# Optimization experiments

Measured on AMD Instinct MI355X. Metric: run time of the kernel, lower is better.

The kernel has to match this reference:

```python
import jax, jax.numpy as jnp
import numpy as np

NEG = -1.0e30  # log-space 'zero' that is safe in fp32
EPS = 1e-7     # keras.backend.ctc_batch_cost epsilon


def setup_inputs() -> dict:
    key = jax.random.key(0)
    k1, k2 = jax.random.split(key)
    B, T, C, L = 256, 512, 256, 128
    # y_pred are post-softmax probabilities, as expected by ctc_batch_cost
    logits = jax.random.normal(k1, (B, T, C), dtype=jnp.float32)
    y_pred = jax.nn.softmax(logits, axis=-1)
    # labels in [0, C-1): never equal to blank index C-1
    y_true = jax.random.randint(k2, (B, L), 0, C - 1, dtype=jnp.int32)
    return {"y_true": y_true, "y_pred": y_pred}


def _ctc_batch_cost(y_true, y_pred):
    """Faithful keras.backend.ctc_batch_cost with full input/label lengths.

    y_true: [B, L] int labels (no blanks). y_pred: [B, T, C] probabilities.
    Blank index = C - 1 (TF v1 ctc_loss convention). Returns [B, 1] loss.
    """
    B, T, C = y_pred.shape
    L = y_true.shape[1]
    blank = C - 1
    S = 2 * L + 1  # extended label: blank, l0, blank, l1, ..., blank

    logp = jnp.log(y_pred + EPS)                                # [B, T, C]
    ext = jnp.full((B, S), blank, dtype=y_true.dtype).at[:, 1::2].set(y_true)
    # per-(t, s) log prob of the extended symbol
    lp = jnp.take_along_axis(logp, ext[:, None, :].astype(jnp.int32), axis=2)  # [B, T, S]

    # skip transition s-2 -> s allowed iff s >= 2, ext[s] != blank, ext[s] != ext[s-2]
    ext_m2 = jnp.pad(ext, ((0, 0), (2, 0)), constant_values=blank)[:, :S]
    skip = (ext != blank) & (ext != ext_m2) & (jnp.arange(S)[None, :] >= 2)

    # alpha init at t=0: only s=0 (blank) and s=1 (first label) reachable
    alpha0 = jnp.where(jnp.arange(S)[None, :] < 2, lp[:, 0, :], NEG)  # [B, S]

    def step(alpha, lp_t):
        p1 = jnp.pad(alpha, ((0, 0), (1, 0)), constant_values=NEG)[:, :S]
        p2 = jnp.pad(alpha, ((0, 0), (2, 0)), constant_values=NEG)[:, :S]
        a = jnp.logaddexp(alpha, p1)
        a = jnp.logaddexp(a, jnp.where(skip, p2, NEG))
        return a + lp_t, None

    lp_time_major = jnp.moveaxis(lp, 1, 0)  # [T, B, S]
    alpha, _ = jax.lax.scan(step, alpha0, lp_time_major[1:])
    # total log-likelihood ends at last blank or last label
    loss = -jnp.logaddexp(alpha[:, S - 1], alpha[:, S - 2])    # [B]
    return loss[:, None]                                        # [B, 1]


def reference(y_true, y_pred):
    # CTCLayer.call computes ctc_batch_cost with input_length = T, label_length = L
    # for every batch row, adds it as a loss, and passes y_pred through. The
    # compute of interest is the loss itself, returned here as [B, 1].
    return _ctc_batch_cost(y_true, y_pred)
```

## Files before the change

kernel.cpp:

```cpp
#include <hip/hip_runtime.h>
#include <math.h>


namespace {
constexpr int Bn = 256;
constexpr int Tn = 512;
constexpr int Cn = 256;
constexpr int Ln = 128;
constexpr int D  = 32;
constexpr float EPSf = 1e-7f;
constexpr float LN2f = 0.69314718055994530942f;
constexpr int   TGT  = 100;
}

typedef float f4 __attribute__((ext_vector_type(4)));

#define GLOAD(dst, p) \
    asm volatile("global_load_dwordx4 %0, %1, off" : "=v"(dst) : "v"(p))
#define WAITP(dst) \
    asm volatile("s_waitcnt vmcnt(31)" : "+v"(dst))
#define WAIT0(dst) \
    asm volatile("s_waitcnt vmcnt(0)" : "+v"(dst))

__device__ __forceinline__ float rdl63(float v) {
    return __int_as_float(__builtin_amdgcn_readlane(__float_as_int(v), 63));
}

__global__ __launch_bounds__(64, 1)
void ctc_fwd(const int* __restrict__ y_true,
             const float* __restrict__ y_pred,
             float* __restrict__ out)
{
    const int b    = blockIdx.x;
    const int lane = threadIdx.x;

    __shared__ __align__(16) float lds[4 * Cn];

    const int* yt = y_true + b * Ln;
    const int l0 = yt[2 * lane];
    const int l1 = yt[2 * lane + 1];
    const int lm = (lane > 0) ? yt[2 * lane - 1] : -1;
    const float sk1 = (lane > 0 && l0 != lm) ? 1.0f : 0.0f;
    const float sk3 = (l1 != l0) ? 1.0f : 0.0f;
    const float lzm = (lane > 0) ? 1.0f : 0.0f;

    float a0 = (lane == 0) ? 0x1p100f : 0.0f;
    float a1 = 0.0f, a2 = 0.0f, a3 = 0.0f, a4 = 0.0f;
    int Eacc = -100;

    auto step = [&](float rb, float r0, float r1) {
        float n = __shfl_up(a3, 1) * lzm;
        const float Pb = rb + EPSf;
        const float P0 = r0 + EPSf;
        const float P1 = r1 + EPSf;
        const float na0 = (a0 + n) * Pb;
        const float na1 = fmaf(sk1, n,  a1 + a0) * P0;
        const float na2 = (a2 + a1) * Pb;
        const float na3 = fmaf(sk3, a1, a3 + a2) * P1;
        const float na4 = (a4 + a3) * Pb;
        a0 = na0; a1 = na1; a2 = na2; a3 = na3; a4 = na4;
    };

    auto rescale = [&]() {
        float m = fmaxf(fmaxf(fmaxf(a0, a1), fmaxf(a2, a3)), a4);
        #pragma unroll
        for (int off = 32; off >= 1; off >>= 1)
            m = fmaxf(m, __shfl_xor(m, off));
        int e;
        (void)frexpf(m, &e);
        const int shift = TGT - e;
        a0 = ldexpf(a0, shift);
        a1 = ldexpf(a1, shift);
        a2 = ldexpf(a2, shift);
        a3 = ldexpf(a3, shift);
        a4 = ldexpf(a4, shift);
        Eacc -= shift;
    };

    const f4* p = (const f4*)(y_pred + (size_t)b * Tn * Cn) + lane;
    f4 buf[D];
    #pragma unroll
    for (int j = 0; j < D; ++j) { GLOAD(buf[j], p); p += Cn / 4; }

    float bold = 0.0f;

    #pragma unroll
    for (int j = 0; j < D; ++j) {
        WAITP(buf[j]);
        const float bnew = rdl63(buf[j].w);
        float r0n = 0.0f, r1n = 0.0f;
        if (j >= 1) {
            r0n = lds[((j - 1) & 3) * Cn + l0];
            r1n = lds[((j - 1) & 3) * Cn + l1];
        }
        ((f4*)lds)[(j & 3) * (Cn / 4) + lane] = buf[j];
        GLOAD(buf[j], p); p += Cn / 4;
        if (j >= 1) step(bold, r0n, r1n);
        bold = bnew;
        if (j == 16) rescale();
    }

    for (int c = D; c < Tn - D; c += D) {
        #pragma unroll
        for (int j = 0; j < D; ++j) {
            WAITP(buf[j]);
            const float bnew = rdl63(buf[j].w);
            const float r0n = lds[((j - 1) & 3) * Cn + l0];
            const float r1n = lds[((j - 1) & 3) * Cn + l1];
            ((f4*)lds)[(j & 3) * (Cn / 4) + lane] = buf[j];
            GLOAD(buf[j], p); p += Cn / 4;
            step(bold, r0n, r1n);
            bold = bnew;
            if (j == 0 || j == 16) rescale();
        }
    }

    #pragma unroll
    for (int j = 0; j < D; ++j) {
        WAIT0(buf[j]);
        const float bnew = rdl63(buf[j].w);
        const float r0n = lds[((j - 1) & 3) * Cn + l0];
        const float r1n = lds[((j - 1) & 3) * Cn + l1];
        ((f4*)lds)[(j & 3) * (Cn / 4) + lane] = buf[j];
        step(bold, r0n, r1n);
        bold = bnew;
        if (j == 0 || j == 16) rescale();
    }

    {
        const float r0n = lds[3 * Cn + l0];
        const float r1n = lds[3 * Cn + l1];
        step(bold, r0n, r1n);
    }

    if (lane == 63) {
        const float s = a3 + a4;
        out[b] = -LN2f * (log2f(s) + (float)Eacc);
    }
}

extern "C" void kernel_launch(void* const* d_in, const int* in_sizes, int n_in,
                              void* d_out, int out_size, void* d_ws, size_t ws_size,
                              hipStream_t stream) {
    const int*   y_true = (const int*)  d_in[0];
    const float* y_pred = (const float*)d_in[1];
    float* out = (float*)d_out;
    (void)in_sizes; (void)n_in; (void)out_size; (void)d_ws; (void)ws_size;
    ctc_fwd<<<dim3(Bn), dim3(64), 0, stream>>>(y_true, y_pred, out);
}
```

Before: 198.6 us.

## Use DPP for lane shifts and reductions, deepen LDS read pipeline by one step

Replaces the __shfl_up neighbor exchange with a DPP wave_shr:1 move that has bound_ctrl zeroing, so lane 0 gets zero without a mask multiply. Replaces the shfl_xor max reduction in rescale with DPP row_shr and row_bcast steps followed by a readlane. Adds one extra step of software pipelining so LDS gathers and the blank-probability readlane are consumed one iteration later, which hides LDS latency from the serial recurrence. This adds a register queue and an extra step in the epilogue, and depends on the DPP bcast semantics being correct on gfx950.

After: 197.8 us. Within noise of the previous version (-0.4%).

```diff
diff --git a/kernel.cpp b/kernel.cpp
--- a/kernel.cpp
+++ b/kernel.cpp
@@ -25,6 +25,16 @@
 __device__ __forceinline__ float rdl63(float v) {
     return __int_as_float(__builtin_amdgcn_readlane(__float_as_int(v), 63));
 }
+__device__ __forceinline__ float dpp_shr1(float v) {
+    return __int_as_float(__builtin_amdgcn_update_dpp(
+        0, __float_as_int(v), 0x138, 0xF, 0xF, true));
+}
+template <int CTRL>
+__device__ __forceinline__ float dpp_max(float m) {
+    float o = __int_as_float(__builtin_amdgcn_update_dpp(
+        0, __float_as_int(m), CTRL, 0xF, 0xF, true));
+    return fmaxf(m, o);
+}
 
 __global__ __launch_bounds__(64, 1)
 void ctc_fwd(const int* __restrict__ y_true,
@@ -42,14 +52,13 @@
     const int lm = (lane > 0) ? yt[2 * lane - 1] : -1;
     const float sk1 = (lane > 0 && l0 != lm) ? 1.0f : 0.0f;
     const float sk3 = (l1 != l0) ? 1.0f : 0.0f;
-    const float lzm = (lane > 0) ? 1.0f : 0.0f;
 
     float a0 = (lane == 0) ? 0x1p100f : 0.0f;
     float a1 = 0.0f, a2 = 0.0f, a3 = 0.0f, a4 = 0.0f;
     int Eacc = -100;
 
     auto step = [&](float rb, float r0, float r1) {
-        float n = __shfl_up(a3, 1) * lzm;
+        const float n = dpp_shr1(a3);
         const float Pb = rb + EPSf;
         const float P0 = r0 + EPSf;
         const float P1 = r1 + EPSf;
@@ -63,9 +72,13 @@
 
     auto rescale = [&]() {
         float m = fmaxf(fmaxf(fmaxf(a0, a1), fmaxf(a2, a3)), a4);
-        #pragma unroll
-        for (int off = 32; off >= 1; off >>= 1)
-            m = fmaxf(m, __shfl_xor(m, off));
+        m = dpp_max<0x111>(m);
+        m = dpp_max<0x112>(m);
+        m = dpp_max<0x114>(m);
+        m = dpp_max<0x118>(m);
+        m = dpp_max<0x142>(m);
+        m = dpp_max<0x143>(m);
+        m = rdl63(m);
         int e;
         (void)frexpf(m, &e);
         const int shift = TGT - e;
@@ -82,7 +95,8 @@
     #pragma unroll
     for (int j = 0; j < D; ++j) { GLOAD(buf[j], p); p += Cn / 4; }
 
-    float bold = 0.0f;
+    float bq0 = 0.0f, bq1 = 0.0f;
+    float r0c = 0.0f, r1c = 0.0f;
 
     #pragma unroll
     for (int j = 0; j < D; ++j) {
@@ -95,9 +109,9 @@
         }
         ((f4*)lds)[(j & 3) * (Cn / 4) + lane] = buf[j];
         GLOAD(buf[j], p); p += Cn / 4;
-        if (j >= 1) step(bold, r0n, r1n);
-        bold = bnew;
-        if (j == 16) rescale();
+        if (j >= 2) step(bq0, r0c, r1c);
+        bq0 = bq1; bq1 = bnew; r0c = r0n; r1c = r1n;
+        if (j == 17) rescale();
     }
 
     for (int c = D; c < Tn - D; c += D) {
@@ -109,9 +123,9 @@
             const float r1n = lds[((j - 1) & 3) * Cn + l1];
             ((f4*)lds)[(j & 3) * (Cn / 4) + lane] = buf[j];
             GLOAD(buf[j], p); p += Cn / 4;
-            step(bold, r0n, r1n);
-            bold = bnew;
-            if (j == 0 || j == 16) rescale();
+            step(bq0, r0c, r1c);
+            bq0 = bq1; bq1 = bnew; r0c = r0n; r1c = r1n;
+            if (j == 1 || j == 17) rescale();
         }
     }
 
@@ -122,15 +136,17 @@
         const float r0n = lds[((j - 1) & 3) * Cn + l0];
         const float r1n = lds[((j - 1) & 3) * Cn + l1];
         ((f4*)lds)[(j & 3) * (Cn / 4) + lane] = buf[j];
-        step(bold, r0n, r1n);
-        bold = bnew;
-        if (j == 0 || j == 16) rescale();
+        step(bq0, r0c, r1c);
+        bq0 = bq1; bq1 = bnew; r0c = r0n; r1c = r1n;
+        if (j == 1 || j == 17) rescale();
     }
 
     {
         const float r0n = lds[3 * Cn + l0];
         const float r1n = lds[3 * Cn + l1];
-        step(bold, r0n, r1n);
+        step(bq0, r0c, r1c);
+        bq0 = bq1; r0c = r0n; r1c = r1n;
+        step(bq0, r0c, r1c);
     }
 
     if (lane == 63) {
```
